# Optimization experiments

Measured on AMD Instinct MI355X. Metric: run time of the kernel, lower is better.

## Reference

```python
import jax, jax.numpy as jnp
import numpy as np

T = 2048        # flattened tokens (one prefill sequence)
HID = 2048      # hidden_size
NH = 32         # query heads
NKV = 4         # kv heads
HD = 128        # head_dim
THETA = 1000000.0
EPS = 1e-6


def setup_inputs() -> dict:
    key = jax.random.key(0)
    k0, k1, k2 = jax.random.split(key, 3)
    return {
        "positions": jnp.arange(T, dtype=jnp.int32),
        "hidden_states": jax.random.normal(k0, (T, HID), dtype=jnp.float32),
        "w_qkv": jax.random.normal(k1, ((NH + 2 * NKV) * HD, HID), dtype=jnp.float32) * 0.02,
        "w_o": jax.random.normal(k2, (HID, NH * HD), dtype=jnp.float32) * 0.02,
        "q_norm_w": jnp.ones((HD,), dtype=jnp.float32),
        "k_norm_w": jnp.ones((HD,), dtype=jnp.float32),
    }


def _rmsnorm(x, w):
    # per-head RMSNorm over last dim (head_dim), fp32 math
    var = jnp.mean(x * x, axis=-1, keepdims=True)
    return x * jax.lax.rsqrt(var + EPS) * w


def _rope(x, positions):
    # NeoX-style rotary embedding over full head_dim
    d = x.shape[-1]
    inv_freq = 1.0 / (THETA ** (jnp.arange(0, d, 2, dtype=jnp.float32) / d))  # [d/2]
    ang = positions.astype(jnp.float32)[:, None] * inv_freq                   # [T, d/2]
    cos = jnp.cos(ang)[:, None, :]  # [T,1,d/2]
    sin = jnp.sin(ang)[:, None, :]
    x1, x2 = jnp.split(x, 2, axis=-1)
    return jnp.concatenate([x1 * cos - x2 * sin, x2 * cos + x1 * sin], axis=-1)


def reference(positions, hidden_states, w_qkv, w_o, q_norm_w, k_norm_w):
    # fused QKV projection (no bias)
    qkv = hidden_states @ w_qkv.T                       # [T, (NH+2*NKV)*HD]
    q, k, v = jnp.split(qkv, [NH * HD, (NH + NKV) * HD], axis=-1)
    q = _rmsnorm(q.reshape(T, NH, HD), q_norm_w)        # [T,NH,HD]
    k = _rmsnorm(k.reshape(T, NKV, HD), k_norm_w)       # [T,NKV,HD]
    v = v.reshape(T, NKV, HD)
    q = _rope(q, positions)
    k = _rope(k, positions)
    # GQA: expand kv heads to query heads
    g = NH // NKV
    k = jnp.repeat(k, g, axis=1)                        # [T,NH,HD]
    v = jnp.repeat(v, g, axis=1)
    scale = HD ** -0.5
    scores = jnp.einsum('qhd,khd->hqk', q, k) * scale   # [NH,T,T]
    causal = jnp.tril(jnp.ones((T, T), dtype=bool))
    scores = jnp.where(causal[None, :, :], scores, jnp.finfo(scores.dtype).min)
    attn = jax.nn.softmax(scores, axis=-1)
    o = jnp.einsum('hqk,khd->qhd', attn, v).reshape(T, NH * HD)
    return o @ w_o.T                                    # [T,HID]
```

## Files before the change

kernel.cpp:

```cpp
#include <hip/hip_runtime.h>
#include <math.h>

#define T 2048
#define HID 2048
#define NH 32
#define NKV 4
#define HD 128
#define QKV_DIM 5120
#define OD 4096
#define C2LOG 0.12751743f
#define MFIX 6.0f

typedef _Float16 half8 __attribute__((ext_vector_type(8)));
typedef _Float16 half4v __attribute__((ext_vector_type(4)));
typedef float floatx4 __attribute__((ext_vector_type(4)));

#define GLD16(gp, lp) __builtin_amdgcn_global_load_lds( \
    (const __attribute__((address_space(1))) void*)(gp), \
    (__attribute__((address_space(3))) void*)(lp), 16, 0, 0)

__global__ __launch_bounds__(256)
void cvt_all(const float* __restrict__ h, const float* __restrict__ wq,
             const float* __restrict__ wo, _Float16* __restrict__ out) {
    size_t i = ((size_t)blockIdx.x * 256 + threadIdx.x) * 4;
    const float* src;
    size_t off;
    if (i < (size_t)T * HID)                        { src = h;  off = i; }
    else if (i < (size_t)T * HID + (size_t)QKV_DIM * HID)
                                                    { src = wq; off = i - (size_t)T * HID; }
    else                                            { src = wo; off = i - (size_t)T * HID - (size_t)QKV_DIM * HID; }
    float4 v = *(const float4*)(src + off);
    half4v o = { (_Float16)v.x, (_Float16)v.y, (_Float16)v.z, (_Float16)v.w };
    *(half4v*)(out + i) = o;
}

__global__ __launch_bounds__(256)
void gemm_sk_h(const _Float16* __restrict__ A, const _Float16* __restrict__ B,
               _Float16* __restrict__ p0, _Float16* __restrict__ p1,
               int M, int N, int K, int KS) {
    __shared__ __align__(16) _Float16 Asm[8192];
    __shared__ __align__(16) _Float16 Bsm[8192];
    int tid = threadIdx.x;
    int wave = tid >> 6, lane = tid & 63;
    int quad = lane >> 4, l16 = lane & 15;
    int m0 = blockIdx.y * 128, n0 = blockIdx.x * 128;
    int koff = blockIdx.z * KS;
    _Float16* C = blockIdx.z ? p1 : p0;
    int wm = (wave >> 1) * 64, wn = (wave & 1) * 64;
    const _Float16* Ag = A + (size_t)(m0 + (tid >> 2)) * K + koff + (tid & 3) * 8;
    const _Float16* Bg = B + (size_t)(n0 + (tid >> 2)) * K + koff + (tid & 3) * 8;
    size_t row64 = (size_t)64 * K;
    _Float16* AsmW = Asm + wave * 512;
    _Float16* BsmW = Bsm + wave * 512;
    floatx4 acc[4][4] = {};
    for (int k0 = 0; k0 < KS; k0 += 64) {
        __syncthreads();
        GLD16(Ag, AsmW);
        GLD16(Ag + row64, AsmW + 2048);
        GLD16(Ag + 32, AsmW + 4096);
        GLD16(Ag + row64 + 32, AsmW + 6144);
        GLD16(Bg, BsmW);
        GLD16(Bg + row64, BsmW + 2048);
        GLD16(Bg + 32, BsmW + 4096);
        GLD16(Bg + row64 + 32, BsmW + 6144);
        Ag += 64; Bg += 64;
        __syncthreads();
        #pragma unroll
        for (int p = 0; p < 2; p++) {
            half8 af[4], bf[4];
            #pragma unroll
            for (int i = 0; i < 4; i++)
                af[i] = *(const half8*)&Asm[p * 4096 + (wm + i * 16 + l16) * 32 + quad * 8];
            #pragma unroll
            for (int j = 0; j < 4; j++)
                bf[j] = *(const half8*)&Bsm[p * 4096 + (wn + j * 16 + l16) * 32 + quad * 8];
            #pragma unroll
            for (int i = 0; i < 4; i++)
                #pragma unroll
                for (int j = 0; j < 4; j++)
                    acc[i][j] = __builtin_amdgcn_mfma_f32_16x16x32_f16(af[i], bf[j], acc[i][j], 0, 0, 0);
        }
    }
    #pragma unroll
    for (int i = 0; i < 4; i++) {
        int row = m0 + wm + i * 16 + quad * 4;
        #pragma unroll
        for (int j = 0; j < 4; j++) {
            int col = n0 + wn + j * 16 + l16;
            #pragma unroll
            for (int r = 0; r < 4; r++)
                C[(size_t)(row + r) * N + col] = (_Float16)acc[i][j][r];
        }
    }
}

__global__ __launch_bounds__(256)
void gemm_sk_f(const _Float16* __restrict__ A, const _Float16* __restrict__ B,
               _Float16* __restrict__ p0, _Float16* __restrict__ p1,
               _Float16* __restrict__ p2, _Float16* __restrict__ p3,
               int M, int N, int K, int KS) {
    __shared__ __align__(16) _Float16 Asm[8192];
    __shared__ __align__(16) _Float16 Bsm[8192];
    int tid = threadIdx.x;
    int wave = tid >> 6, lane = tid & 63;
    int quad = lane >> 4, l16 = lane & 15;
    int m0 = blockIdx.y * 128, n0 = blockIdx.x * 128;
    int bz = blockIdx.z;
    int koff = bz * KS;
    _Float16* C = (bz == 0) ? p0 : (bz == 1) ? p1 : (bz == 2) ? p2 : p3;
    int wm = (wave >> 1) * 64, wn = (wave & 1) * 64;
    const _Float16* Ag = A + (size_t)(m0 + (tid >> 2)) * K + koff + (tid & 3) * 8;
    const _Float16* Bg = B + (size_t)(n0 + (tid >> 2)) * K + koff + (tid & 3) * 8;
    size_t row64 = (size_t)64 * K;
    _Float16* AsmW = Asm + wave * 512;
    _Float16* BsmW = Bsm + wave * 512;
    floatx4 acc[4][4] = {};
    for (int k0 = 0; k0 < KS; k0 += 64) {
        __syncthreads();
        GLD16(Ag, AsmW);
        GLD16(Ag + row64, AsmW + 2048);
        GLD16(Ag + 32, AsmW + 4096);
        GLD16(Ag + row64 + 32, AsmW + 6144);
        GLD16(Bg, BsmW);
        GLD16(Bg + row64, BsmW + 2048);
        GLD16(Bg + 32, BsmW + 4096);
        GLD16(Bg + row64 + 32, BsmW + 6144);
        Ag += 64; Bg += 64;
        __syncthreads();
        #pragma unroll
        for (int p = 0; p < 2; p++) {
            half8 af[4], bf[4];
            #pragma unroll
            for (int i = 0; i < 4; i++)
                af[i] = *(const half8*)&Asm[p * 4096 + (wm + i * 16 + l16) * 32 + quad * 8];
            #pragma unroll
            for (int j = 0; j < 4; j++)
                bf[j] = *(const half8*)&Bsm[p * 4096 + (wn + j * 16 + l16) * 32 + quad * 8];
            #pragma unroll
            for (int i = 0; i < 4; i++)
                #pragma unroll
                for (int j = 0; j < 4; j++)
                    acc[i][j] = __builtin_amdgcn_mfma_f32_16x16x32_f16(af[i], bf[j], acc[i][j], 0, 0, 0);
        }
    }
    #pragma unroll
    for (int i = 0; i < 4; i++) {
        int row = m0 + wm + i * 16 + quad * 4;
        #pragma unroll
        for (int j = 0; j < 4; j++) {
            int col = n0 + wn + j * 16 + l16;
            #pragma unroll
            for (int r = 0; r < 4; r++)
                C[(size_t)(row + r) * N + col] = (_Float16)acc[i][j][r];
        }
    }
}

__global__ __launch_bounds__(256)
void reduce4(const _Float16* __restrict__ p0, const _Float16* __restrict__ p1,
             const _Float16* __restrict__ p2, const _Float16* __restrict__ p3,
             float* __restrict__ out) {
    size_t i = ((size_t)blockIdx.x * 256 + threadIdx.x) * 4;
    half4v a = *(const half4v*)(p0 + i);
    half4v b = *(const half4v*)(p1 + i);
    half4v c = *(const half4v*)(p2 + i);
    half4v d = *(const half4v*)(p3 + i);
    float4 o = { (float)a.x + (float)b.x + (float)c.x + (float)d.x,
                 (float)a.y + (float)b.y + (float)c.y + (float)d.y,
                 (float)a.z + (float)b.z + (float)c.z + (float)d.z,
                 (float)a.w + (float)b.w + (float)c.w + (float)d.w };
    *(float4*)(out + i) = o;
}

__global__ __launch_bounds__(256)
void qkv_post(const _Float16* __restrict__ qp0, const _Float16* __restrict__ qp1,
              const int* __restrict__ positions,
              const float* __restrict__ qw, const float* __restrict__ kw,
              _Float16* __restrict__ Qb, _Float16* __restrict__ Kb,
              _Float16* __restrict__ Vt) {
    int t = blockIdx.x;
    int wave = threadIdx.x >> 6, lane = threadIdx.x & 63;
    float pos = (float)positions[t];
    float f = exp2f(-(float)lane * (19.9315685693241741f / 64.0f));
    float ang = pos * f;
    float s = sinf(ang), c = cosf(ang);
    const _Float16* r0 = qp0 + (size_t)t * QKV_DIM;
    const _Float16* r1 = qp1 + (size_t)t * QKV_DIM;
    for (int hh = wave; hh < NH + 2 * NKV; hh += 4) {
        float x1 = (float)r0[hh * HD + lane] + (float)r1[hh * HD + lane];
        float x2 = (float)r0[hh * HD + lane + 64] + (float)r1[hh * HD + lane + 64];
        if (hh < NH + NKV) {
            float ss = x1 * x1 + x2 * x2;
            for (int o = 1; o < 64; o <<= 1) ss += __shfl_xor(ss, o);
            float inv = rsqrtf(ss * (1.0f / HD) + 1e-6f);
            const float* w = (hh < NH) ? qw : kw;
            x1 = x1 * inv * w[lane];
            x2 = x2 * inv * w[lane + 64];
            float y1 = x1 * c - x2 * s;
            float y2 = x2 * c + x1 * s;
            _Float16* dst;
            if (hh < NH) dst = Qb + ((size_t)hh * T + t) * HD;
            else         dst = Kb + ((size_t)(hh - NH) * T + t) * HD;
            dst[lane]      = (_Float16)y1;
            dst[lane + 64] = (_Float16)y2;
        } else {
            int hk = hh - NH - NKV;
            Vt[((size_t)hk * HD + lane) * T + t]      = (_Float16)x1;
            Vt[((size_t)hk * HD + lane + 64) * T + t] = (_Float16)x2;
        }
    }
}

__global__ __launch_bounds__(256, 4)
void attn(const _Float16* __restrict__ Qb, const _Float16* __restrict__ Kb,
          const _Float16* __restrict__ Vt, _Float16* __restrict__ Ob) {
    __shared__ __align__(16) _Float16 Ksm[8192];
    __shared__ __align__(16) _Float16 Vsm[8192];
    __shared__ __align__(16) _Float16 Psm[4][1024];
    int b = blockIdx.x;
    int h = b & 31;
    int quarter = b >> 8;
    int i = (b & 255) >> 5;
    int qt = (quarter == 0) ? 31 - i : (quarter == 1) ? i
           : (quarter == 2) ? 23 - i : 8 + i;
    int hk = h >> 3;
    int tid = threadIdx.x, wave = tid >> 6, lane = tid & 63;
    int quad = lane >> 4, l16 = lane & 15;
    int q0 = qt * 64;
    int wbase = q0 + wave * 16;

    half8 aq[4];
    {
        const _Float16* qp = Qb + ((size_t)h * T + wbase + l16) * HD + quad * 8;
        #pragma unroll
        for (int dk = 0; dk < 4; dk++)
            aq[dk] = *(const half8*)(qp + dk * 32);
    }
    floatx4 o_acc[8] = {};
    float lpart[4] = {};

    int krow = tid >> 4;
    const _Float16* Kg = Kb + ((size_t)hk * T + krow) * HD + ((tid & 15) ^ (krow & 7)) * 8;
    int vrow = tid >> 3;
    const _Float16* Vg = Vt + ((size_t)hk * HD + vrow) * T + ((tid & 7) ^ (vrow & 7)) * 8;
    _Float16* KsmW = Ksm + wave * 512;
    _Float16* VsmW = Vsm + wave * 512;
    _Float16* PsmW = Psm[wave];

    int ntiles = qt + 1;
    for (int it = 0; it < ntiles; it++) {
        int kv0 = it * 64;
        __syncthreads();
        {
            const _Float16* kg = Kg + (size_t)kv0 * HD;
            const _Float16* vg = Vg + kv0;
            #pragma unroll
            for (int c = 0; c < 4; c++) {
                GLD16(kg + (size_t)c * (16 * HD), KsmW + c * 2048);
                GLD16(vg + (size_t)c * (32 * T), VsmW + c * 2048);
            }
        }
        __syncthreads();

        floatx4 sfr[4];
        #pragma unroll
        for (int sn = 0; sn < 4; sn++) {
            int row = sn * 16 + l16;
            int rs = row & 7;
            floatx4 a = {};
            #pragma unroll
            for (int dk = 0; dk < 4; dk++) {
                half8 kf = *(const half8*)&Ksm[row * 128 + ((dk * 4 + quad) ^ rs) * 8];
                a = __builtin_amdgcn_mfma_f32_16x16x32_f16(aq[dk], kf, a, 0, 0, 0);
            }
            sfr[sn] = a;
        }

        bool needmask = (it == ntiles - 1);
        int rq = wbase + quad * 4;
        #pragma unroll
        for (int sn = 0; sn < 4; sn++) {
            int kv = kv0 + sn * 16 + l16;
            #pragma unroll
            for (int r = 0; r < 4; r++) {
                float p = __builtin_amdgcn_exp2f(
                    __builtin_fmaf(sfr[sn][r], C2LOG, -MFIX));
                if (needmask) p = (kv <= rq + r) ? p : 0.0f;
                lpart[r] += p;
                int prow = quad * 4 + r;
                int cb = sn * 2 + (l16 >> 3);
                PsmW[prow * 64 + ((cb ^ (prow & 7)) * 8 + (l16 & 7))] = (_Float16)p;
            }
        }
        half8 ap0 = *(const half8*)&PsmW[l16 * 64 + ((quad ^ (l16 & 7)) * 8)];
        half8 ap1 = *(const half8*)&PsmW[l16 * 64 + (((4 + quad) ^ (l16 & 7)) * 8)];

        #pragma unroll
        for (int dn = 0; dn < 8; dn++) {
            int row = dn * 16 + l16;
            int rs = row & 7;
            half8 v0 = *(const half8*)&Vsm[row * 64 + ((quad ^ rs) * 8)];
            half8 v1 = *(const half8*)&Vsm[row * 64 + (((4 + quad) ^ rs) * 8)];
            o_acc[dn] = __builtin_amdgcn_mfma_f32_16x16x32_f16(ap0, v0, o_acc[dn], 0, 0, 0);
            o_acc[dn] = __builtin_amdgcn_mfma_f32_16x16x32_f16(ap1, v1, o_acc[dn], 0, 0, 0);
        }
    }

    #pragma unroll
    for (int o = 1; o < 16; o <<= 1)
        #pragma unroll
        for (int r = 0; r < 4; r++)
            lpart[r] += __shfl_xor(lpart[r], o);
    float linv[4];
    #pragma unroll
    for (int r = 0; r < 4; r++) linv[r] = 1.0f / lpart[r];
    int rowb = wbase + quad * 4;
    #pragma unroll
    for (int dn = 0; dn < 8; dn++) {
        int col = h * HD + dn * 16 + l16;
        #pragma unroll
        for (int r = 0; r < 4; r++)
            Ob[(size_t)(rowb + r) * OD + col] = (_Float16)(o_acc[dn][r] * linv[r]);
    }
}

extern "C" void kernel_launch(void* const* d_in, const int* in_sizes, int n_in,
                              void* d_out, int out_size, void* d_ws, size_t ws_size,
                              hipStream_t stream) {
    const int*   positions = (const int*)d_in[0];
    const float* hidden    = (const float*)d_in[1];
    const float* w_qkv     = (const float*)d_in[2];
    const float* w_o       = (const float*)d_in[3];
    const float* q_norm_w  = (const float*)d_in[4];
    const float* k_norm_w  = (const float*)d_in[5];
    float* out = (float*)d_out;

    const size_t MiB = 1048576;
    char* ws = (char*)d_ws;
    _Float16* hb    = (_Float16*)(ws);
    _Float16* wqkvb = (_Float16*)(ws + 8 * MiB);
    _Float16* wob   = (_Float16*)(ws + 28 * MiB);
    _Float16* qkvp0 = (_Float16*)(ws + 44 * MiB);
    _Float16* qkvp1 = (_Float16*)(ws + 64 * MiB);
    _Float16* Qb    = (_Float16*)(ws + 84 * MiB);
    _Float16* Kb    = (_Float16*)(ws + 100 * MiB);
    _Float16* Vt    = (_Float16*)(ws + 102 * MiB);
    _Float16* Ob    = (_Float16*)(ws + 104 * MiB);
    _Float16* op0   = (_Float16*)(ws);
    _Float16* op1   = (_Float16*)(ws + 9 * MiB);
    _Float16* op2   = (_Float16*)(ws + 44 * MiB);
    _Float16* op3   = (_Float16*)(ws + 53 * MiB);

    cvt_all<<<22528, 256, 0, stream>>>(hidden, w_qkv, w_o, hb);

    gemm_sk_h<<<dim3(QKV_DIM / 128, T / 128, 2), 256, 0, stream>>>(
        hb, wqkvb, qkvp0, qkvp1, T, QKV_DIM, HID, HID / 2);

    qkv_post<<<T, 256, 0, stream>>>(qkvp0, qkvp1, positions, q_norm_w, k_norm_w, Qb, Kb, Vt);

    attn<<<1024, 256, 0, stream>>>(Qb, Kb, Vt, Ob);

    gemm_sk_f<<<dim3(HID / 128, T / 128, 4), 256, 0, stream>>>(
        Ob, wob, op0, op1, op2, op3, T, HID, OD, OD / 4);
    reduce4<<<T * HID / 1024, 256, 0, stream>>>(op0, op1, op2, op3, out);
}
```

Measured before the change: 332.2 us.

## Prefetch next K/V tile into registers during attention compute, add MFMA priority

```diff
diff --git a/kernel.cpp b/kernel.cpp
--- a/kernel.cpp
+++ b/kernel.cpp
@@ -246,23 +246,40 @@
     _Float16* KsmW = Ksm + wave * 512;
     _Float16* VsmW = Vsm + wave * 512;
     _Float16* PsmW = Psm[wave];
+    _Float16* Kw = KsmW + (size_t)lane * 8;
+    _Float16* Vw = VsmW + (size_t)lane * 8;
 
     int ntiles = qt + 1;
+
+    half8 kst[4], vst[4];
+    #pragma unroll
+    for (int c = 0; c < 4; c++) {
+        kst[c] = *(const half8*)(Kg + (size_t)c * (16 * HD));
+        vst[c] = *(const half8*)(Vg + (size_t)c * (32 * T));
+    }
+
     for (int it = 0; it < ntiles; it++) {
         int kv0 = it * 64;
-        __syncthreads();
-        {
-            const _Float16* kg = Kg + (size_t)kv0 * HD;
-            const _Float16* vg = Vg + kv0;
+        __builtin_amdgcn_s_barrier();
+        #pragma unroll
+        for (int c = 0; c < 4; c++) {
+            *(half8*)(Kw + c * 2048) = kst[c];
+            *(half8*)(Vw + c * 2048) = vst[c];
+        }
+        if (it + 1 < ntiles) {
+            int kv0n = kv0 + 64;
             #pragma unroll
             for (int c = 0; c < 4; c++) {
-                GLD16(kg + (size_t)c * (16 * HD), KsmW + c * 2048);
-                GLD16(vg + (size_t)c * (32 * T), VsmW + c * 2048);
+                kst[c] = *(const half8*)(Kg + (size_t)kv0n * HD + (size_t)c * (16 * HD));
+                vst[c] = *(const half8*)(Vg + kv0n + (size_t)c * (32 * T));
             }
         }
-        __syncthreads();
+        asm volatile("s_waitcnt lgkmcnt(0)" ::: "memory");
+        __builtin_amdgcn_s_barrier();
+        __builtin_amdgcn_sched_barrier(0);
 
         floatx4 sfr[4];
+        __builtin_amdgcn_s_setprio(1);
         #pragma unroll
         for (int sn = 0; sn < 4; sn++) {
             int row = sn * 16 + l16;
@@ -275,6 +292,7 @@
             }
             sfr[sn] = a;
         }
+        __builtin_amdgcn_s_setprio(0);
 
         bool needmask = (it == ntiles - 1);
         int rq = wbase + quad * 4;
@@ -295,6 +313,7 @@
         half8 ap0 = *(const half8*)&PsmW[l16 * 64 + ((quad ^ (l16 & 7)) * 8)];
         half8 ap1 = *(const half8*)&PsmW[l16 * 64 + (((4 + quad) ^ (l16 & 7)) * 8)];
 
+        __builtin_amdgcn_s_setprio(1);
         #pragma unroll
         for (int dn = 0; dn < 8; dn++) {
             int row = dn * 16 + l16;
@@ -304,6 +323,7 @@
             o_acc[dn] = __builtin_amdgcn_mfma_f32_16x16x32_f16(ap0, v0, o_acc[dn], 0, 0, 0);
             o_acc[dn] = __builtin_amdgcn_mfma_f32_16x16x32_f16(ap1, v1, o_acc[dn], 0, 0, 0);
         }
+        __builtin_amdgcn_s_setprio(0);
     }
 
     #pragma unroll
```

Result: slower. 394.8 us (+18.8%).

## Double-buffer LDS tiles in split-K GEMMs to overlap global loads with MFMA

Applied to the files above, without the earlier changes.

```diff
diff --git a/kernel.cpp b/kernel.cpp
--- a/kernel.cpp
+++ b/kernel.cpp
@@ -50,36 +50,43 @@
     const _Float16* Ag = A + (size_t)(m0 + (tid >> 2)) * K + koff + (tid & 3) * 8;
     const _Float16* Bg = B + (size_t)(n0 + (tid >> 2)) * K + koff + (tid & 3) * 8;
     size_t row64 = (size_t)64 * K;
-    _Float16* AsmW = Asm + wave * 512;
-    _Float16* BsmW = Bsm + wave * 512;
+    int wofs = wave * 512;
     floatx4 acc[4][4] = {};
-    for (int k0 = 0; k0 < KS; k0 += 64) {
-        __syncthreads();
-        GLD16(Ag, AsmW);
-        GLD16(Ag + row64, AsmW + 2048);
-        GLD16(Ag + 32, AsmW + 4096);
-        GLD16(Ag + row64 + 32, AsmW + 6144);
-        GLD16(Bg, BsmW);
-        GLD16(Bg + row64, BsmW + 2048);
-        GLD16(Bg + 32, BsmW + 4096);
-        GLD16(Bg + row64 + 32, BsmW + 6144);
-        Ag += 64; Bg += 64;
-        __syncthreads();
-        #pragma unroll
-        for (int p = 0; p < 2; p++) {
-            half8 af[4], bf[4];
-            #pragma unroll
-            for (int i = 0; i < 4; i++)
-                af[i] = *(const half8*)&Asm[p * 4096 + (wm + i * 16 + l16) * 32 + quad * 8];
+    int nt = KS >> 5;
+    GLD16(Ag, Asm + wofs);
+    GLD16(Ag + row64, Asm + 2048 + wofs);
+    GLD16(Bg, Bsm + wofs);
+    GLD16(Bg + row64, Bsm + 2048 + wofs);
+    for (int t = 0; t < nt; t++) {
+        int cur = t & 1;
+        if (t + 1 < nt) {
+            const _Float16* Agp = Ag + (size_t)(t + 1) * 32;
+            const _Float16* Bgp = Bg + (size_t)(t + 1) * 32;
+            int nb = (cur ^ 1) * 4096 + wofs;
+            GLD16(Agp, Asm + nb);
+            GLD16(Agp + row64, Asm + nb + 2048);
+            GLD16(Bgp, Bsm + nb);
+            GLD16(Bgp + row64, Bsm + nb + 2048);
+            asm volatile("s_waitcnt vmcnt(4)" ::: "memory");
+        } else {
+            asm volatile("s_waitcnt vmcnt(0)" ::: "memory");
+        }
+        __builtin_amdgcn_s_barrier();
+        __builtin_amdgcn_sched_barrier(0);
+        int pb = cur * 4096;
+        half8 af[4], bf[4];
+        #pragma unroll
+        for (int i = 0; i < 4; i++)
+            af[i] = *(const half8*)&Asm[pb + (wm + i * 16 + l16) * 32 + quad * 8];
+        #pragma unroll
+        for (int j = 0; j < 4; j++)
+            bf[j] = *(const half8*)&Bsm[pb + (wn + j * 16 + l16) * 32 + quad * 8];
+        #pragma unroll
+        for (int i = 0; i < 4; i++)
             #pragma unroll
             for (int j = 0; j < 4; j++)
-                bf[j] = *(const half8*)&Bsm[p * 4096 + (wn + j * 16 + l16) * 32 + quad * 8];
-            #pragma unroll
-            for (int i = 0; i < 4; i++)
-                #pragma unroll
-                for (int j = 0; j < 4; j++)
-                    acc[i][j] = __builtin_amdgcn_mfma_f32_16x16x32_f16(af[i], bf[j], acc[i][j], 0, 0, 0);
-        }
+                acc[i][j] = __builtin_amdgcn_mfma_f32_16x16x32_f16(af[i], bf[j], acc[i][j], 0, 0, 0);
+        __builtin_amdgcn_s_barrier();
     }
     #pragma unroll
     for (int i = 0; i < 4; i++) {
@@ -112,36 +119,43 @@
     const _Float16* Ag = A + (size_t)(m0 + (tid >> 2)) * K + koff + (tid & 3) * 8;
     const _Float16* Bg = B + (size_t)(n0 + (tid >> 2)) * K + koff + (tid & 3) * 8;
     size_t row64 = (size_t)64 * K;
-    _Float16* AsmW = Asm + wave * 512;
-    _Float16* BsmW = Bsm + wave * 512;
+    int wofs = wave * 512;
     floatx4 acc[4][4] = {};
-    for (int k0 = 0; k0 < KS; k0 += 64) {
-        __syncthreads();
-        GLD16(Ag, AsmW);
-        GLD16(Ag + row64, AsmW + 2048);
-        GLD16(Ag + 32, AsmW + 4096);
-        GLD16(Ag + row64 + 32, AsmW + 6144);
-        GLD16(Bg, BsmW);
-        GLD16(Bg + row64, BsmW + 2048);
-        GLD16(Bg + 32, BsmW + 4096);
-        GLD16(Bg + row64 + 32, BsmW + 6144);
-        Ag += 64; Bg += 64;
-        __syncthreads();
-        #pragma unroll
-        for (int p = 0; p < 2; p++) {
-            half8 af[4], bf[4];
-            #pragma unroll
-            for (int i = 0; i < 4; i++)
-                af[i] = *(const half8*)&Asm[p * 4096 + (wm + i * 16 + l16) * 32 + quad * 8];
+    int nt = KS >> 5;
+    GLD16(Ag, Asm + wofs);
+    GLD16(Ag + row64, Asm + 2048 + wofs);
+    GLD16(Bg, Bsm + wofs);
+    GLD16(Bg + row64, Bsm + 2048 + wofs);
+    for (int t = 0; t < nt; t++) {
+        int cur = t & 1;
+        if (t + 1 < nt) {
+            const _Float16* Agp = Ag + (size_t)(t + 1) * 32;
+            const _Float16* Bgp = Bg + (size_t)(t + 1) * 32;
+            int nb = (cur ^ 1) * 4096 + wofs;
+            GLD16(Agp, Asm + nb);
+            GLD16(Agp + row64, Asm + nb + 2048);
+            GLD16(Bgp, Bsm + nb);
+            GLD16(Bgp + row64, Bsm + nb + 2048);
+            asm volatile("s_waitcnt vmcnt(4)" ::: "memory");
+        } else {
+            asm volatile("s_waitcnt vmcnt(0)" ::: "memory");
+        }
+        __builtin_amdgcn_s_barrier();
+        __builtin_amdgcn_sched_barrier(0);
+        int pb = cur * 4096;
+        half8 af[4], bf[4];
+        #pragma unroll
+        for (int i = 0; i < 4; i++)
+            af[i] = *(const half8*)&Asm[pb + (wm + i * 16 + l16) * 32 + quad * 8];
+        #pragma unroll
+        for (int j = 0; j < 4; j++)
+            bf[j] = *(const half8*)&Bsm[pb + (wn + j * 16 + l16) * 32 + quad * 8];
+        #pragma unroll
+        for (int i = 0; i < 4; i++)
             #pragma unroll
             for (int j = 0; j < 4; j++)
-                bf[j] = *(const half8*)&Bsm[p * 4096 + (wn + j * 16 + l16) * 32 + quad * 8];
-            #pragma unroll
-            for (int i = 0; i < 4; i++)
-                #pragma unroll
-                for (int j = 0; j < 4; j++)
-                    acc[i][j] = __builtin_amdgcn_mfma_f32_16x16x32_f16(af[i], bf[j], acc[i][j], 0, 0, 0);
-        }
+                acc[i][j] = __builtin_amdgcn_mfma_f32_16x16x32_f16(af[i], bf[j], acc[i][j], 0, 0, 0);
+        __builtin_amdgcn_s_barrier();
     }
     #pragma unroll
     for (int i = 0; i < 4; i++) {
```

After: 330.3 us. Within noise of the previous version (-0.6%).
